# Optimization experiments

Hardware: AMD Instinct MI355X
Metric: run time of the kernel (lower is better)

## Reference

```python
import jax, jax.numpy as jnp
import numpy as np

NEG_SLOPE = 0.1

def mlp(x, w1, b1, w2, b2):
    # MLP(sizes): Linear -> LeakyReLU(0.1) -> Linear
    return jax.nn.leaky_relu(x @ w1 + b1, NEG_SLOPE) @ w2 + b2

def _seg_mean(vals, idx, n):
    s = jax.ops.segment_sum(vals, idx, num_segments=n)
    cnt = jax.ops.segment_sum(jnp.ones((vals.shape[0],), vals.dtype), idx, num_segments=n)
    return s / jnp.maximum(cnt, 1.0)[:, None]

def setup_inputs() -> dict:
    key = jax.random.key(0)
    ks = iter(jax.random.split(key, 40))
    N, F, H, E = 100000, 64, 128, 800000
    Ha = H // 2  # hidden_dim/2 = 64
    def lin(k, i, o):
        k1, k2 = jax.random.split(k)
        return (jax.random.normal(k1, (i, o), jnp.float32) * (1.0 / np.sqrt(i)),
                jax.random.normal(k2, (o,), jnp.float32) * 0.01)
    inp = {}
    inp['feat'] = jax.random.normal(next(ks), (N, F), jnp.float32)
    inp['pi_feat'] = jax.random.normal(next(ks), (N, 4), jnp.float32)
    inp['level'] = jax.random.uniform(next(ks), (N, 1), jnp.float32)
    inp['bit_position'] = jax.random.uniform(next(ks), (E, 1), jnp.float32)
    inp['is_po'] = jax.random.randint(next(ks), (N,), 0, 2, jnp.int32)
    inp['is_module'] = jax.random.randint(next(ks), (N,), 0, 2, jnp.int32)
    inp['src_m'] = jax.random.randint(next(ks), (E,), 0, N, jnp.int32)
    inp['dst_m'] = jax.random.randint(next(ks), (E,), 0, N, jnp.int32)
    inp['src_g'] = jax.random.randint(next(ks), (E,), 0, N, jnp.int32)
    inp['dst_g'] = jax.random.randint(next(ks), (E,), 0, N, jnp.int32)
    # mlp_pi: 4 -> H/2 -> H
    inp['pi_w1'], inp['pi_b1'] = lin(next(ks), 4, Ha)
    inp['pi_w2'], inp['pi_b2'] = lin(next(ks), Ha, H)
    # mlp_neigh_module: H + F + 1 -> H/2 -> H
    inp['nm_w1'], inp['nm_b1'] = lin(next(ks), H + F + 1, Ha)
    inp['nm_w2'], inp['nm_b2'] = lin(next(ks), Ha, H)
    # mlp_neigh_gate: H + F -> H/2 -> H
    inp['ng_w1'], inp['ng_b1'] = lin(next(ks), H + F, Ha)
    inp['ng_w2'], inp['ng_b2'] = lin(next(ks), Ha, H)
    # mlp_global: 1 -> H/2 -> H
    inp['g_w1'], inp['g_b1'] = lin(next(ks), 1, Ha)
    inp['g_w2'], inp['g_b2'] = lin(next(ks), Ha, H)
    # mlp_out: 2H -> H -> 1
    inp['o_w1'], inp['o_b1'] = lin(next(ks), 2 * H, H)
    inp['o_w2'], inp['o_b2'] = lin(next(ks), H, 1)
    return inp

def reference(feat, pi_feat, level, bit_position,
              pi_w1, pi_b1, pi_w2, pi_b2,
              nm_w1, nm_b1, nm_w2, nm_b2,
              ng_w1, ng_b1, ng_w2, ng_b2,
              g_w1, g_b1, g_w2, g_b2,
              o_w1, o_b1, o_w2, o_b2,
              is_po, is_module, src_m, dst_m, src_g, dst_g):
    N = feat.shape[0]
    # PI init embedding (mlp_pi)
    h0 = mlp(pi_feat, pi_w1, pi_b1, pi_w2, pi_b2)            # [N, H]
    # module-edge message passing: m = src h, pos = bit_position; mean reduce
    m = h0[src_m]                                            # [E, H] irregular gather
    neigh_m = _seg_mean(m, dst_m, N)                         # [N, H]
    pos_m = _seg_mean(bit_position, dst_m, N)                # [N, 1]
    # nodes_func_module, agg_choice==0: cat(neigh, pos, feat) -> mlp_neigh_module
    h_m = mlp(jnp.concatenate([neigh_m, pos_m, feat], axis=1), nm_w1, nm_b1, nm_w2, nm_b2)
    # gate-edge message passing
    neigh_g = _seg_mean(h0[src_g], dst_g, N)                 # [N, H]
    h_g = mlp(jnp.concatenate([neigh_g, feat], axis=1), ng_w1, ng_b1, ng_w2, ng_b2)
    # ReLU on non-PO nodes only
    keep = (is_po != 1)[:, None]
    h_m = jnp.where(keep, jax.nn.relu(h_m), h_m)
    h_g = jnp.where(keep, jax.nn.relu(h_g), h_g)
    # per-node-type update (hetero apply_nodes)
    h = jnp.where((is_module == 1)[:, None], h_m, h_g)       # [N, H]
    # global branch + readout
    hg = mlp(level, g_w1, g_b1, g_w2, g_b2)                  # [N, H]
    out = mlp(jnp.concatenate([h, hg], axis=1), o_w1, o_b1, o_w2, o_b2)  # [N, 1]
    return out
```

## Files before the change

### kernel.cpp

```cpp
#include <hip/hip_runtime.h>

typedef __bf16 bf16x8 __attribute__((ext_vector_type(8)));
typedef float f32x4 __attribute__((ext_vector_type(4)));
typedef unsigned short u16;
typedef unsigned int u32;
typedef unsigned long long u64;

__device__ __forceinline__ u16 f2b(float f) {
  return __builtin_bit_cast(u16, (__bf16)f);
}
__device__ __forceinline__ float b2f_lo(u32 pk) {
  return __builtin_bit_cast(float, pk << 16);
}
__device__ __forceinline__ float b2f_hi(u32 pk) {
  return __builtin_bit_cast(float, pk & 0xffff0000u);
}
__device__ __forceinline__ float leaky(float x) { return x > 0.f ? x : 0.1f * x; }
__device__ __forceinline__ f32x4 mfma16(bf16x8 a, bf16x8 b, f32x4 c) {
  return __builtin_amdgcn_mfma_f32_16x16x32_bf16(a, b, c, 0, 0, 0);
}

#define P64 72
#define P128 136
#define CAP 16
#define RSTRIDE 32

#define PREPB 32
#define SBLK 256
#define PBLK 224

__global__ __launch_bounds__(256) void k_init(
    const float* nm_w1, const float* ng_w1, const float* pi_w2, const float* pi_b2,
    const int* is_module,
    u16* wt_yc, float* bias_y, u16* wt_f1m, u16* wt_f1g,
    int* rec, int* spillcnt, u32* mbits, int N) {
  int i = blockIdx.x * 256 + threadIdx.x;
  if (i < 9216) {
    int ty = i / 4608, rem = i % 4608, n = rem / P64, k = rem % P64;
    float v = 0.f;
    if (k < 64) {
      const float* w1 = ty ? ng_w1 : nm_w1;
      for (int t = 0; t < 128; t++) v += pi_w2[k * 128 + t] * w1[t * 64 + n];
    }
    wt_yc[i] = f2b(v);
    return;
  }
  i -= 9216;
  if (i < 128) {
    int ty = i >> 6, n = i & 63;
    const float* w1 = ty ? ng_w1 : nm_w1;
    float v = 0.f;
    for (int t = 0; t < 128; t++) v += pi_b2[t] * w1[t * 64 + n];
    bias_y[i] = v;
    return;
  }
  i -= 128;
  if (i < 4608) {
    int n = i / P64, k = i % P64;
    wt_f1m[i] = f2b(k < 64 ? nm_w1[(129 + k) * 64 + n] : 0.f);
    return;
  }
  i -= 4608;
  if (i < 4608) {
    int n = i / P64, k = i % P64;
    wt_f1g[i] = f2b(k < 64 ? ng_w1[(128 + k) * 64 + n] : 0.f);
    return;
  }
  i -= 4608;
  {
    int n = i;
    int lane = threadIdx.x & 63;
    bool v = (n < N) && (is_module[n] == 1);
    u64 b = __ballot(v);
    if (n < N) {
      rec[(size_t)n * RSTRIDE] = 0;
      rec[(size_t)n * RSTRIDE + 1] = 0;
      if (lane == 0) mbits[n >> 5] = (u32)b;
      if (lane == 32) mbits[n >> 5] = (u32)(b >> 32);
    }
    if (n == 0) *spillcnt = 0;
  }
}

__global__ __launch_bounds__(512) void k_mid(
    const int* src_m, const int* dst_m, const int* src_g, const int* dst_g,
    const u32* mbits, const float* bitpos, int* rec, u64* spill, int* spillcnt,
    int E,
    const float* pf, const float* feat, const float* pi_w1, const float* pi_b1,
    const u16* wt_yc_g, const float* bias_y, const u16* wt_f1m_g, const u16* wt_f1g_g,
    const float* nm_b1, const float* ng_b1, u16* y0, u16* f1,
    const float* nm_w1, const float* nm_w2, const float* ng_w2,
    const float* o_w1, const float* o_b1, const float* g_w2, const float* g_b2,
    u16* wt2m, u16* wt2g, u16* wt_oh, u16* gt, float* bp, float* w_pos, int N) {
  __shared__ __align__(16) u16 wyc[2][64 * P64];
  __shared__ __align__(16) u16 wf[2][64 * P64];
  __shared__ __align__(16) u16 tbuf[8][16 * P64];

  if (blockIdx.x < PREPB) {
    const int TOTAL = 9216 + 9216 + 17408 + 9216 + 128 + 64;
    for (int it = blockIdx.x * 512 + threadIdx.x; it < TOTAL; it += PREPB * 512) {
      int i = it;
      if (i < 9216) {
        int n = i / P64, k = i % P64;
        wt2m[i] = f2b(k < 64 ? nm_w2[k * 128 + n] : 0.f);
        continue;
      }
      i -= 9216;
      if (i < 9216) {
        int n = i / P64, k = i % P64;
        wt2g[i] = f2b(k < 64 ? ng_w2[k * 128 + n] : 0.f);
        continue;
      }
      i -= 9216;
      if (i < 17408) {
        int n = i / P128, k = i % P128;
        wt_oh[i] = f2b(k < 128 ? o_w1[k * 128 + n] : 0.f);
        continue;
      }
      i -= 17408;
      if (i < 9216) {
        int n = i / P64, k = i % P64;
        float v = 0.f;
        if (k < 64)
          for (int t = 0; t < 128; t++) v += g_w2[k * 128 + t] * o_w1[(128 + t) * 128 + n];
        gt[i] = f2b(v);
        continue;
      }
      i -= 9216;
      if (i < 128) {
        float s = o_b1[i];
        for (int t = 0; t < 128; t++) s += g_b2[t] * o_w1[(128 + t) * 128 + i];
        bp[i] = s;
        continue;
      }
      i -= 128;
      w_pos[i] = nm_w1[128 * 64 + i];
    }
    return;
  }

  if (blockIdx.x < PREPB + SBLK) {
    int tid = (blockIdx.x - PREPB) * 512 + threadIdx.x;
    const int STR = SBLK * 512;
    for (int v0 = tid; v0 < E; v0 += STR * 4) {
      int dd[8], ss[8];
      float bb[8];
      bool el[8];
#pragma unroll
      for (int k = 0; k < 4; k++) {
        int vt = v0 + k * STR;
        bool vv = vt < E;
#pragma unroll
        for (int j = 0; j < 2; j++) {
          int x = k * 2 + j;
          el[x] = false;
          dd[x] = 0; ss[x] = 0; bb[x] = 0.f;
          if (vv) {
            int e = vt * 2 + j;
            int d = (e < E) ? dst_m[e] : dst_g[e - E];
            dd[x] = d;
            bool bit = (mbits[d >> 5] >> (d & 31)) & 1;
            el[x] = (e < E) ? bit : !bit;
            if (el[x]) {
              if (e < E) { ss[x] = src_m[e]; bb[x] = bitpos[e]; }
              else ss[x] = src_g[e - E];
            }
          }
        }
      }
      int cc[8];
#pragma unroll
      for (int x = 0; x < 8; x++)
        if (el[x]) cc[x] = atomicAdd(&rec[(size_t)dd[x] * RSTRIDE], 1);
#pragma unroll
      for (int x = 0; x < 8; x++) {
        if (!el[x]) continue;
        int vt = v0 + (x >> 1) * STR;
        int e = vt * 2 + (x & 1);
        int d = dd[x], s = ss[x], c = cc[x];
        if (e < E) {
          if (c < CAP) {
            int bp12 = (int)(bb[x] * 4096.f);
            if (bp12 > 4095) bp12 = 4095;
            rec[(size_t)d * RSTRIDE + 2 + c] = (s << 12) | bp12;
          } else {
            int p = atomicAdd(spillcnt, 1);
            spill[p] = ((u64)(u32)d << 32) | (u32)s;
            atomicAdd((float*)&rec[(size_t)d * RSTRIDE + 1], bb[x]);
          }
        } else {
          if (c < CAP) {
            rec[(size_t)d * RSTRIDE + 2 + c] = s << 12;
          } else {
            int p = atomicAdd(spillcnt, 1);
            spill[p] = ((u64)(u32)d << 32) | (u32)s;
          }
        }
      }
    }
    return;
  }

  int pb = blockIdx.x - PREPB - SBLK;
  for (int i = threadIdx.x; i < 2304; i += 512) {
    ((u32*)wyc[0])[i] = ((const u32*)wt_yc_g)[i];
    ((u32*)wyc[1])[i] = ((const u32*)wt_yc_g)[2304 + i];
    ((u32*)wf[0])[i] = ((const u32*)wt_f1m_g)[i];
    ((u32*)wf[1])[i] = ((const u32*)wt_f1g_g)[i];
  }

  int lane = threadIdx.x & 63, wv = threadIdx.x >> 6;
  int lid = lane & 15, q = lane >> 4;

  bf16x8 w1f[4];
#pragma unroll
  for (int nt = 0; nt < 4; nt++) {
    bf16x8 f;
#pragma unroll
    for (int j = 0; j < 8; j++) {
      int k = q * 8 + j;
      f[j] = (__bf16)((k < 4) ? pi_w1[k * 64 + nt * 16 + lid] : 0.f);
    }
    w1f[nt] = f;
  }
  __syncthreads();

  int nbat = (N + 15) >> 4;
  for (int b0 = pb * 8; b0 < nbat; b0 += PBLK * 8) {
    int b = b0 + wv;
    int batch = b < nbat ? b : nbat - 1;
    int id = batch * 16 + lid;
    if (id >= N) id = N - 1;

    bf16x8 a;
#pragma unroll
    for (int j = 0; j < 8; j++)
      a[j] = (__bf16)((q == 0 && j < 4) ? pf[(size_t)id * 4 + j] : 0.f);
    f32x4 z1[4];
#pragma unroll
    for (int nt = 0; nt < 4; nt++) {
      f32x4 c = {0.f, 0.f, 0.f, 0.f};
      z1[nt] = mfma16(a, w1f[nt], c);
    }
    __syncthreads();
#pragma unroll
    for (int nt = 0; nt < 4; nt++) {
      float bb = pi_b1[nt * 16 + lid];
#pragma unroll
      for (int r = 0; r < 4; r++)
        tbuf[wv][(q * 4 + r) * P64 + nt * 16 + lid] = f2b(leaky(z1[nt][r] + bb));
    }
    __syncthreads();
    bf16x8 a20 = *(const bf16x8*)&tbuf[wv][lid * P64 + q * 8];
    bf16x8 a21 = *(const bf16x8*)&tbuf[wv][lid * P64 + 32 + q * 8];

    int idr_[4];
#pragma unroll
    for (int r = 0; r < 4; r++) {
      int ii = batch * 16 + q * 4 + r;
      idr_[r] = ii < N ? ii : N - 1;
    }

#pragma unroll
    for (int ty = 0; ty < 2; ty++) {
#pragma unroll
      for (int nt = 0; nt < 4; nt++) {
        f32x4 c = {0.f, 0.f, 0.f, 0.f};
        c = mfma16(a20, *(const bf16x8*)&wyc[ty][(nt * 16 + lid) * P64 + q * 8], c);
        c = mfma16(a21, *(const bf16x8*)&wyc[ty][(nt * 16 + lid) * P64 + 32 + q * 8], c);
        float by = bias_y[ty * 64 + nt * 16 + lid];
#pragma unroll
        for (int r = 0; r < 4; r++)
          y0[(size_t)idr_[r] * 128 + ty * 64 + nt * 16 + lid] = f2b(c[r] + by);
      }
    }

    bf16x8 af[2];
#pragma unroll
    for (int kt = 0; kt < 2; kt++) {
      const float4* p = (const float4*)(feat + (size_t)id * 64 + kt * 32 + q * 8);
      float4 xa = p[0], xb = p[1];
      bf16x8 f;
      f[0] = (__bf16)xa.x; f[1] = (__bf16)xa.y; f[2] = (__bf16)xa.z; f[3] = (__bf16)xa.w;
      f[4] = (__bf16)xb.x; f[5] = (__bf16)xb.y; f[6] = (__bf16)xb.z; f[7] = (__bf16)xb.w;
      af[kt] = f;
    }
#pragma unroll
    for (int nt = 0; nt < 4; nt++) {
      f32x4 cm = {0.f, 0.f, 0.f, 0.f}, cg = {0.f, 0.f, 0.f, 0.f};
#pragma unroll
      for (int kt = 0; kt < 2; kt++) {
        cm = mfma16(af[kt], *(const bf16x8*)&wf[0][(nt * 16 + lid) * P64 + kt * 32 + q * 8], cm);
        cg = mfma16(af[kt], *(const bf16x8*)&wf[1][(nt * 16 + lid) * P64 + kt * 32 + q * 8], cg);
      }
      float bm = nm_b1[nt * 16 + lid], bg = ng_b1[nt * 16 + lid];
#pragma unroll
      for (int r = 0; r < 4; r++) {
        int idr = idr_[r];
        bool mod = (mbits[idr >> 5] >> (idr & 31)) & 1;
        f1[(size_t)idr * 64 + nt * 16 + lid] = f2b(mod ? cm[r] + bm : cg[r] + bg);
      }
    }
  }
}

__global__ __launch_bounds__(256) void k_gather(const u16* y0, const int* rec,
                                                const u64* spill, const int* spillcnt,
                                                const u32* mbits, const u16* f1,
                                                const float* w_pos, u16* z1a, int N) {
  int n = (blockIdx.x * 256 + threadIdx.x) >> 6;
  int lane = threadIdx.x & 63;
  if (n >= N) return;
  bool mod = (mbits[n >> 5] >> (n & 31)) & 1;
  int g = lane >> 4, l16 = lane & 15;
  int rv = (lane < 18) ? rec[(size_t)n * RSTRIDE + lane] : 0;
  int cnt = __shfl(rv, 0);
  float pspill = __builtin_bit_cast(float, __shfl(rv, 1));
  int inl = cnt < CAP ? cnt : CAP;
  float myb = 0.f;
  if (mod && lane >= 2 && lane < 18 && (lane - 2) < inl)
    myb = (float)(rv & 4095) * (1.f / 4096.f);
  const u32* yrow = (const u32*)y0;
  int halfo = mod ? 0 : 32;
  float a00 = 0.f, a01 = 0.f, a10 = 0.f, a11 = 0.f;
  for (int j = 0; j < inl; j += 4) {
    int e = j + g;
    if (e < inl) {
      int s = (int)(((u32)__shfl(rv, 2 + e)) >> 12);
      u64 pk = *(const u64*)(yrow + (size_t)s * 64 + halfo + 2 * l16);
      u32 p0 = (u32)pk, p1 = (u32)(pk >> 32);
      a00 += b2f_lo(p0); a01 += b2f_hi(p0);
      a10 += b2f_lo(p1); a11 += b2f_hi(p1);
    }
  }
  if (cnt > CAP) {
    int sc = *spillcnt;
    int idx = 0;
    for (int base = 0; base < sc; base += 64) {
      int i = base + lane;
      u64 ent = (i < sc) ? spill[i] : 0xffffffffffffffffull;
      bool m = ((int)(ent >> 32) == n);
      u64 bal = __ballot(m);
      int slo = (int)(ent & 0xffffffffu);
      while (bal) {
        int l = __ffsll((long long)bal) - 1;
        bal &= bal - 1;
        int s = __shfl(slo, l);
        if ((idx & 3) == g) {
          u64 pk = *(const u64*)(yrow + (size_t)s * 64 + halfo + 2 * l16);
          u32 p0 = (u32)pk, p1 = (u32)(pk >> 32);
          a00 += b2f_lo(p0); a01 += b2f_hi(p0);
          a10 += b2f_lo(p1); a11 += b2f_hi(p1);
        }
        idx++;
      }
    }
  }
  a00 += __shfl_xor(a00, 16); a00 += __shfl_xor(a00, 32);
  a01 += __shfl_xor(a01, 16); a01 += __shfl_xor(a01, 32);
  a10 += __shfl_xor(a10, 16); a10 += __shfl_xor(a10, 32);
  a11 += __shfl_xor(a11, 16); a11 += __shfl_xor(a11, 32);
#pragma unroll
  for (int off = 1; off < 64; off <<= 1) myb += __shfl_xor(myb, off);
  float psum = pspill + myb;
  float inv = 1.f / (float)(cnt > 1 ? cnt : 1);
  if (lane < 16) {
    u64 fp2 = *(const u64*)(((const u32*)f1) + (size_t)n * 32 + 2 * l16);
    u32 f0 = (u32)fp2, f1v = (u32)(fp2 >> 32);
    float z00 = a00 * inv + b2f_lo(f0);
    float z01 = a01 * inv + b2f_hi(f0);
    float z10 = a10 * inv + b2f_lo(f1v);
    float z11 = a11 * inv + b2f_hi(f1v);
    if (mod) {
      float pm = psum * inv;
      float4 wp = ((const float4*)w_pos)[l16];
      z00 += pm * wp.x; z01 += pm * wp.y;
      z10 += pm * wp.z; z11 += pm * wp.w;
    }
    u32 r0 = (u32)f2b(leaky(z00)) | ((u32)f2b(leaky(z01)) << 16);
    u32 r1 = (u32)f2b(leaky(z10)) | ((u32)f2b(leaky(z11)) << 16);
    *(u64*)(((u32*)z1a) + (size_t)n * 32 + 2 * l16) = ((u64)r1 << 32) | r0;
  }
}

__global__ __launch_bounds__(512) void k_tail(const u16* z1a, const u16* wt2m_g,
                                              const u16* wt2g_g, const float* nm_b2,
                                              const float* ng_b2, const u32* mbits,
                                              const int* is_po, const float* level,
                                              const float* g_w1, const float* g_b1,
                                              const u16* wt_oh_g, const u16* gt_g,
                                              const float* bp_g, const float* o_w2,
                                              const float* o_b2, float* out, int N) {
  __shared__ __align__(16) u16 w2[2][128 * P64];
  __shared__ __align__(16) u16 wt_oh[128 * P128];
  __shared__ __align__(16) u16 gt[128 * P64];
  __shared__ __align__(16) u16 tbuf[8][16 * P128];
  for (int i = threadIdx.x; i < 128 * P64 / 2; i += 512) {
    ((u32*)w2[0])[i] = ((const u32*)wt2m_g)[i];
    ((u32*)w2[1])[i] = ((const u32*)wt2g_g)[i];
    ((u32*)gt)[i] = ((const u32*)gt_g)[i];
  }
  for (int i = threadIdx.x; i < 128 * P128 / 2; i += 512)
    ((u32*)wt_oh)[i] = ((const u32*)wt_oh_g)[i];

  int lane = threadIdx.x & 63, wv = threadIdx.x >> 6;
  int lid = lane & 15, q = lane >> 4;
  int nbat = (N + 15) >> 4;

  float gw[2][8], gb[2][8];
#pragma unroll
  for (int kt = 0; kt < 2; kt++)
#pragma unroll
    for (int j = 0; j < 8; j++) {
      int k = kt * 32 + q * 8 + j;
      gw[kt][j] = g_w1[k];
      gb[kt][j] = g_b1[k];
    }
  float w2o[8], bpv[8];
#pragma unroll
  for (int nt = 0; nt < 8; nt++) {
    w2o[nt] = o_w2[nt * 16 + lid];
    bpv[nt] = bp_g[nt * 16 + lid];
  }
  float b2m[8], b2g[8];
#pragma unroll
  for (int nt = 0; nt < 8; nt++) {
    b2m[nt] = nm_b2[nt * 16 + lid];
    b2g[nt] = ng_b2[nt * 16 + lid];
  }
  float ob2 = o_b2[0];
  __syncthreads();

  for (int b0 = blockIdx.x * 8; b0 < nbat; b0 += gridDim.x * 8) {
    int b = b0 + wv;
    int batch = b < nbat ? b : nbat - 1;
    int id = batch * 16 + lid;
    if (id >= N) id = N - 1;

    bf16x8 a0 = *(const bf16x8*)(z1a + (size_t)id * 64 + q * 8);
    bf16x8 a1 = *(const bf16x8*)(z1a + (size_t)id * 64 + 32 + q * 8);
    bool mod_[4], kp_[4];
#pragma unroll
    for (int r = 0; r < 4; r++) {
      int ii = batch * 16 + q * 4 + r;
      if (ii >= N) ii = N - 1;
      mod_[r] = (mbits[ii >> 5] >> (ii & 31)) & 1;
      kp_[r] = (is_po[ii] != 1);
    }
    __syncthreads();
#pragma unroll
    for (int nt = 0; nt < 8; nt++) {
      f32x4 cm = {0.f, 0.f, 0.f, 0.f}, cg = {0.f, 0.f, 0.f, 0.f};
      cm = mfma16(a0, *(const bf16x8*)&w2[0][(nt * 16 + lid) * P64 + q * 8], cm);
      cm = mfma16(a1, *(const bf16x8*)&w2[0][(nt * 16 + lid) * P64 + 32 + q * 8], cm);
      cg = mfma16(a0, *(const bf16x8*)&w2[1][(nt * 16 + lid) * P64 + q * 8], cg);
      cg = mfma16(a1, *(const bf16x8*)&w2[1][(nt * 16 + lid) * P64 + 32 + q * 8], cg);
#pragma unroll
      for (int r = 0; r < 4; r++) {
        float v = mod_[r] ? cm[r] + b2m[nt] : cg[r] + b2g[nt];
        if (kp_[r]) v = fmaxf(v, 0.f);
        tbuf[wv][(q * 4 + r) * P128 + nt * 16 + lid] = f2b(v);
      }
    }
    __syncthreads();

    bf16x8 ah[4];
#pragma unroll
    for (int kt = 0; kt < 4; kt++)
      ah[kt] = *(const bf16x8*)&tbuf[wv][lid * P128 + kt * 32 + q * 8];
    float lv = level[id];
    bf16x8 ag[2];
#pragma unroll
    for (int kt = 0; kt < 2; kt++)
#pragma unroll
      for (int j = 0; j < 8; j++)
        ag[kt][j] = (__bf16)leaky(lv * gw[kt][j] + gb[kt][j]);

    f32x4 accv[8];
#pragma unroll
    for (int nt = 0; nt < 8; nt++) {
      f32x4 c = {0.f, 0.f, 0.f, 0.f};
#pragma unroll
      for (int kt = 0; kt < 4; kt++)
        c = mfma16(ah[kt], *(const bf16x8*)&wt_oh[(nt * 16 + lid) * P128 + kt * 32 + q * 8], c);
#pragma unroll
      for (int kt = 0; kt < 2; kt++)
        c = mfma16(ag[kt], *(const bf16x8*)&gt[(nt * 16 + lid) * P64 + kt * 32 + q * 8], c);
      accv[nt] = c;
    }
    float p[4];
#pragma unroll
    for (int r = 0; r < 4; r++) {
      float s = 0.f;
#pragma unroll
      for (int nt = 0; nt < 8; nt++) s += leaky(accv[nt][r] + bpv[nt]) * w2o[nt];
      p[r] = s;
    }
#pragma unroll
    for (int r = 0; r < 4; r++)
#pragma unroll
      for (int off = 1; off < 16; off <<= 1) p[r] += __shfl_xor(p[r], off, 16);
    if (lid == 0) {
#pragma unroll
      for (int r = 0; r < 4; r++) {
        int idr = batch * 16 + q * 4 + r;
        if (idr >= N) idr = N - 1;
        out[idr] = p[r] + ob2;
      }
    }
  }
}

extern "C" void kernel_launch(void* const* d_in, const int* in_sizes, int n_in,
                              void* d_out, int out_size, void* d_ws, size_t ws_size,
                              hipStream_t stream) {
  const float* feat = (const float*)d_in[0];
  const float* pi_feat = (const float*)d_in[1];
  const float* level = (const float*)d_in[2];
  const float* bitpos = (const float*)d_in[3];
  const int* is_po = (const int*)d_in[4];
  const int* is_module = (const int*)d_in[5];
  const int* src_m = (const int*)d_in[6];
  const int* dst_m = (const int*)d_in[7];
  const int* src_g = (const int*)d_in[8];
  const int* dst_g = (const int*)d_in[9];
  const float* pi_w1 = (const float*)d_in[10];
  const float* pi_b1 = (const float*)d_in[11];
  const float* pi_w2 = (const float*)d_in[12];
  const float* pi_b2 = (const float*)d_in[13];
  const float* nm_w1 = (const float*)d_in[14];
  const float* nm_b1 = (const float*)d_in[15];
  const float* nm_w2 = (const float*)d_in[16];
  const float* nm_b2 = (const float*)d_in[17];
  const float* ng_w1 = (const float*)d_in[18];
  const float* ng_b1 = (const float*)d_in[19];
  const float* ng_w2 = (const float*)d_in[20];
  const float* ng_b2 = (const float*)d_in[21];
  const float* g_w1 = (const float*)d_in[22];
  const float* g_b1 = (const float*)d_in[23];
  const float* g_w2 = (const float*)d_in[24];
  const float* g_b2 = (const float*)d_in[25];
  const float* o_w1 = (const float*)d_in[26];
  const float* o_b1 = (const float*)d_in[27];
  const float* o_w2 = (const float*)d_in[28];
  const float* o_b2 = (const float*)d_in[29];

  int N = in_sizes[0] / 64;
  int E = in_sizes[3];

  char* ws = (char*)d_ws;
  size_t off = 0;
  auto alloc = [&](size_t bytes) {
    char* p = ws + off;
    off += (bytes + 255) & ~(size_t)255;
    return p;
  };
  int* rec = (int*)alloc(((size_t)N * RSTRIDE + 64) * 4);
  int* spillcnt = (int*)alloc(16);
  u64* spill = (u64*)alloc((size_t)2 * E * 8);
  u32* mbits = (u32*)alloc((size_t)((N + 31) / 32) * 4);
  u16* y0 = (u16*)alloc((size_t)N * 128 * 2);
  u16* f1 = (u16*)alloc((size_t)N * 64 * 2);
  u16* z1a = (u16*)alloc((size_t)N * 64 * 2);
  u16* wt_yc = (u16*)alloc(9216 * 2);
  float* bias_y = (float*)alloc(128 * 4);
  u16* wt_f1m = (u16*)alloc(4608 * 2);
  u16* wt_f1g = (u16*)alloc(4608 * 2);
  float* w_pos = (float*)alloc(64 * 4);
  u16* wt2m = (u16*)alloc(9216 * 2);
  u16* wt2g = (u16*)alloc(9216 * 2);
  u16* wt_oh = (u16*)alloc(17408 * 2);
  u16* gt = (u16*)alloc(9216 * 2);
  float* bp = (float*)alloc(128 * 4);

  int init_items = 18560 + ((N + 63) & ~63);
  k_init<<<(init_items + 255) / 256, 256, 0, stream>>>(
      nm_w1, ng_w1, pi_w2, pi_b2, is_module,
      wt_yc, bias_y, wt_f1m, wt_f1g, rec, spillcnt, mbits, N);

  k_mid<<<PREPB + SBLK + PBLK, 512, 0, stream>>>(
      src_m, dst_m, src_g, dst_g, mbits, bitpos, rec, spill, spillcnt, E,
      pi_feat, feat, pi_w1, pi_b1, wt_yc, bias_y, wt_f1m, wt_f1g,
      nm_b1, ng_b1, y0, f1,
      nm_w1, nm_w2, ng_w2, o_w1, o_b1, g_w2, g_b2,
      wt2m, wt2g, wt_oh, gt, bp, w_pos, N);

  k_gather<<<(N * 64 + 255) / 256, 256, 0, stream>>>(
      y0, rec, spill, spillcnt, mbits, f1, w_pos, z1a, N);

  k_tail<<<256, 512, 0, stream>>>(z1a, wt2m, wt2g, nm_b2, ng_b2, mbits, is_po,
                                  level, g_w1, g_b1, wt_oh, gt, bp, o_w2, o_b2,
                                  (float*)d_out, N);
}
```

Before: 260.9 us.

## Fuse neighbor gather into tail kernel, keeping z1 activations in LDS

Merges the gather/mean-aggregation kernel into the tail MLP kernel. Each wave now gathers 16 nodes at once, with 4 lanes per node and 16-byte loads, and writes the first-layer activations to a per-wave LDS buffer instead of the z1a global array. It also removes the block-wide __syncthreads inside the loop, since each wave only touches its own LDS slices. This drops one launch and the z1a write and read-back. In exchange, gather parallelism is limited to the tail kernel's 256 persistent blocks, which may expose gather latency, and LDS use goes up, which may lower occupancy.

```diff
diff --git a/kernel.cpp b/kernel.cpp
--- a/kernel.cpp
+++ b/kernel.cpp
@@ -304,97 +304,18 @@
   }
 }
 
-__global__ __launch_bounds__(256) void k_gather(const u16* y0, const int* rec,
-                                                const u64* spill, const int* spillcnt,
-                                                const u32* mbits, const u16* f1,
-                                                const float* w_pos, u16* z1a, int N) {
-  int n = (blockIdx.x * 256 + threadIdx.x) >> 6;
-  int lane = threadIdx.x & 63;
-  if (n >= N) return;
-  bool mod = (mbits[n >> 5] >> (n & 31)) & 1;
-  int g = lane >> 4, l16 = lane & 15;
-  int rv = (lane < 18) ? rec[(size_t)n * RSTRIDE + lane] : 0;
-  int cnt = __shfl(rv, 0);
-  float pspill = __builtin_bit_cast(float, __shfl(rv, 1));
-  int inl = cnt < CAP ? cnt : CAP;
-  float myb = 0.f;
-  if (mod && lane >= 2 && lane < 18 && (lane - 2) < inl)
-    myb = (float)(rv & 4095) * (1.f / 4096.f);
-  const u32* yrow = (const u32*)y0;
-  int halfo = mod ? 0 : 32;
-  float a00 = 0.f, a01 = 0.f, a10 = 0.f, a11 = 0.f;
-  for (int j = 0; j < inl; j += 4) {
-    int e = j + g;
-    if (e < inl) {
-      int s = (int)(((u32)__shfl(rv, 2 + e)) >> 12);
-      u64 pk = *(const u64*)(yrow + (size_t)s * 64 + halfo + 2 * l16);
-      u32 p0 = (u32)pk, p1 = (u32)(pk >> 32);
-      a00 += b2f_lo(p0); a01 += b2f_hi(p0);
-      a10 += b2f_lo(p1); a11 += b2f_hi(p1);
-    }
-  }
-  if (cnt > CAP) {
-    int sc = *spillcnt;
-    int idx = 0;
-    for (int base = 0; base < sc; base += 64) {
-      int i = base + lane;
-      u64 ent = (i < sc) ? spill[i] : 0xffffffffffffffffull;
-      bool m = ((int)(ent >> 32) == n);
-      u64 bal = __ballot(m);
-      int slo = (int)(ent & 0xffffffffu);
-      while (bal) {
-        int l = __ffsll((long long)bal) - 1;
-        bal &= bal - 1;
-        int s = __shfl(slo, l);
-        if ((idx & 3) == g) {
-          u64 pk = *(const u64*)(yrow + (size_t)s * 64 + halfo + 2 * l16);
-          u32 p0 = (u32)pk, p1 = (u32)(pk >> 32);
-          a00 += b2f_lo(p0); a01 += b2f_hi(p0);
-          a10 += b2f_lo(p1); a11 += b2f_hi(p1);
-        }
-        idx++;
-      }
-    }
-  }
-  a00 += __shfl_xor(a00, 16); a00 += __shfl_xor(a00, 32);
-  a01 += __shfl_xor(a01, 16); a01 += __shfl_xor(a01, 32);
-  a10 += __shfl_xor(a10, 16); a10 += __shfl_xor(a10, 32);
-  a11 += __shfl_xor(a11, 16); a11 += __shfl_xor(a11, 32);
-#pragma unroll
-  for (int off = 1; off < 64; off <<= 1) myb += __shfl_xor(myb, off);
-  float psum = pspill + myb;
-  float inv = 1.f / (float)(cnt > 1 ? cnt : 1);
-  if (lane < 16) {
-    u64 fp2 = *(const u64*)(((const u32*)f1) + (size_t)n * 32 + 2 * l16);
-    u32 f0 = (u32)fp2, f1v = (u32)(fp2 >> 32);
-    float z00 = a00 * inv + b2f_lo(f0);
-    float z01 = a01 * inv + b2f_hi(f0);
-    float z10 = a10 * inv + b2f_lo(f1v);
-    float z11 = a11 * inv + b2f_hi(f1v);
-    if (mod) {
-      float pm = psum * inv;
-      float4 wp = ((const float4*)w_pos)[l16];
-      z00 += pm * wp.x; z01 += pm * wp.y;
-      z10 += pm * wp.z; z11 += pm * wp.w;
-    }
-    u32 r0 = (u32)f2b(leaky(z00)) | ((u32)f2b(leaky(z01)) << 16);
-    u32 r1 = (u32)f2b(leaky(z10)) | ((u32)f2b(leaky(z11)) << 16);
-    *(u64*)(((u32*)z1a) + (size_t)n * 32 + 2 * l16) = ((u64)r1 << 32) | r0;
-  }
-}
-
-__global__ __launch_bounds__(512) void k_tail(const u16* z1a, const u16* wt2m_g,
-                                              const u16* wt2g_g, const float* nm_b2,
-                                              const float* ng_b2, const u32* mbits,
-                                              const int* is_po, const float* level,
-                                              const float* g_w1, const float* g_b1,
-                                              const u16* wt_oh_g, const u16* gt_g,
-                                              const float* bp_g, const float* o_w2,
-                                              const float* o_b2, float* out, int N) {
+__global__ __launch_bounds__(512) void k_gt2(
+    const u16* y0, const int* rec, const u64* spill, const int* spillcnt,
+    const u32* mbits, const u16* f1, const float* w_pos,
+    const u16* wt2m_g, const u16* wt2g_g, const float* nm_b2, const float* ng_b2,
+    const int* is_po, const float* level, const float* g_w1, const float* g_b1,
+    const u16* wt_oh_g, const u16* gt_g, const float* bp_g, const float* o_w2,
+    const float* o_b2, float* out, int N) {
   __shared__ __align__(16) u16 w2[2][128 * P64];
   __shared__ __align__(16) u16 wt_oh[128 * P128];
   __shared__ __align__(16) u16 gt[128 * P64];
   __shared__ __align__(16) u16 tbuf[8][16 * P128];
+  __shared__ __align__(16) u32 zl[8][16][36];
   for (int i = threadIdx.x; i < 128 * P64 / 2; i += 512) {
     ((u32*)w2[0])[i] = ((const u32*)wt2m_g)[i];
     ((u32*)w2[1])[i] = ((const u32*)wt2g_g)[i];
@@ -405,6 +326,7 @@
 
   int lane = threadIdx.x & 63, wv = threadIdx.x >> 6;
   int lid = lane & 15, q = lane >> 4;
+  int g4 = lane >> 2, c = lane & 3, base4 = lane & ~3;
   int nbat = (N + 15) >> 4;
 
   float gw[2][8], gb[2][8];
@@ -431,14 +353,126 @@
   float ob2 = o_b2[0];
   __syncthreads();
 
+  const u32* yrow = (const u32*)y0;
+
   for (int b0 = blockIdx.x * 8; b0 < nbat; b0 += gridDim.x * 8) {
     int b = b0 + wv;
     int batch = b < nbat ? b : nbat - 1;
+
+    {
+      int n = batch * 16 + g4;
+      if (n >= N) n = N - 1;
+      bool mod = (mbits[n >> 5] >> (n & 31)) & 1;
+      int halfo = mod ? 0 : 32;
+      const int* rbase = rec + (size_t)n * RSTRIDE;
+      int4 r4 = ((const int4*)rbase)[c];
+      int e16 = 0, e17 = 0;
+      if (c == 1) { e16 = rbase[16]; e17 = rbase[17]; }
+      int cnt = __shfl(r4.x, base4);
+      float pspill = __builtin_bit_cast(float, __shfl(r4.y, base4));
+      int inl = cnt < CAP ? cnt : CAP;
+      float myb = 0.f;
+      float alo[8], ahi[8];
+#pragma unroll
+      for (int m = 0; m < 8; m++) { alo[m] = 0.f; ahi[m] = 0.f; }
+#pragma unroll
+      for (int j = 0; j < 16; j++) {
+        int slot;
+        if (j < 14) {
+          const int own = (j + 2) >> 2, comp = (j + 2) & 3;
+          int v = comp == 0 ? r4.x : comp == 1 ? r4.y : comp == 2 ? r4.z : r4.w;
+          slot = __shfl(v, base4 + own);
+        } else {
+          slot = __shfl(j == 14 ? e16 : e17, base4 + 1);
+        }
+        if (j < inl) {
+          if (mod) myb += (float)(slot & 4095) * (1.f / 4096.f);
+          int s = (int)(((u32)slot) >> 12);
+          const u32* rowp = yrow + (size_t)s * 64 + halfo + c * 8;
+          uint4 pa = *(const uint4*)rowp;
+          uint4 pb = *(const uint4*)(rowp + 4);
+          alo[0] += b2f_lo(pa.x); ahi[0] += b2f_hi(pa.x);
+          alo[1] += b2f_lo(pa.y); ahi[1] += b2f_hi(pa.y);
+          alo[2] += b2f_lo(pa.z); ahi[2] += b2f_hi(pa.z);
+          alo[3] += b2f_lo(pa.w); ahi[3] += b2f_hi(pa.w);
+          alo[4] += b2f_lo(pb.x); ahi[4] += b2f_hi(pb.x);
+          alo[5] += b2f_lo(pb.y); ahi[5] += b2f_hi(pb.y);
+          alo[6] += b2f_lo(pb.z); ahi[6] += b2f_hi(pb.z);
+          alo[7] += b2f_lo(pb.w); ahi[7] += b2f_hi(pb.w);
+        }
+      }
+      u64 over = __ballot(c == 0 && cnt > CAP);
+      if (over) {
+        int sc = *spillcnt;
+        while (over) {
+          int bit = __ffsll((long long)over) - 1;
+          over &= over - 1;
+          int gsel = bit >> 2;
+          int n_t = __shfl(n, bit);
+          int halfo_t = __shfl(halfo, bit);
+          for (int bb = 0; bb < sc; bb += 64) {
+            int i = bb + lane;
+            u64 ent = (i < sc) ? spill[i] : 0xffffffffffffffffull;
+            bool m = ((int)(ent >> 32) == n_t);
+            u64 bal = __ballot(m);
+            int slo = (int)(ent & 0xffffffffu);
+            while (bal) {
+              int l = __ffsll((long long)bal) - 1;
+              bal &= bal - 1;
+              int s = __shfl(slo, l);
+              if (g4 == gsel) {
+                const u32* rowp = yrow + (size_t)s * 64 + halfo_t + c * 8;
+                uint4 pa = *(const uint4*)rowp;
+                uint4 pb = *(const uint4*)(rowp + 4);
+                alo[0] += b2f_lo(pa.x); ahi[0] += b2f_hi(pa.x);
+                alo[1] += b2f_lo(pa.y); ahi[1] += b2f_hi(pa.y);
+                alo[2] += b2f_lo(pa.z); ahi[2] += b2f_hi(pa.z);
+                alo[3] += b2f_lo(pa.w); ahi[3] += b2f_hi(pa.w);
+                alo[4] += b2f_lo(pb.x); ahi[4] += b2f_hi(pb.x);
+                alo[5] += b2f_lo(pb.y); ahi[5] += b2f_hi(pb.y);
+                alo[6] += b2f_lo(pb.z); ahi[6] += b2f_hi(pb.z);
+                alo[7] += b2f_lo(pb.w); ahi[7] += b2f_hi(pb.w);
+              }
+            }
+          }
+        }
+      }
+      float psum = pspill + myb;
+      float inv = 1.f / (float)(cnt > 1 ? cnt : 1);
+      float pm = mod ? psum * inv : 0.f;
+      const u32* f1p = ((const u32*)f1) + (size_t)n * 32 + c * 8;
+      uint4 fa = *(const uint4*)f1p;
+      uint4 fb = *(const uint4*)(f1p + 4);
+      const float4* wp4 = (const float4*)w_pos;
+      float4 wpa = wp4[c * 4 + 0], wpb = wp4[c * 4 + 1];
+      float4 wpc = wp4[c * 4 + 2], wpd = wp4[c * 4 + 3];
+      u32 zr[8];
+#pragma unroll
+      for (int m = 0; m < 8; m++) {
+        u32 fw = (m == 0) ? fa.x : (m == 1) ? fa.y : (m == 2) ? fa.z : (m == 3) ? fa.w
+               : (m == 4) ? fb.x : (m == 5) ? fb.y : (m == 6) ? fb.z : fb.w;
+        float z0 = alo[m] * inv + b2f_lo(fw);
+        float z1v = ahi[m] * inv + b2f_hi(fw);
+        if (mod) {
+          float4 w4 = ((m >> 1) == 0) ? wpa : ((m >> 1) == 1) ? wpb
+                    : ((m >> 1) == 2) ? wpc : wpd;
+          float wx = (m & 1) ? w4.z : w4.x;
+          float wy = (m & 1) ? w4.w : w4.y;
+          z0 += pm * wx;
+          z1v += pm * wy;
+        }
+        zr[m] = (u32)f2b(leaky(z0)) | ((u32)f2b(leaky(z1v)) << 16);
+      }
+      u32* zp = &zl[wv][g4][c * 8];
+      *(uint4*)zp = make_uint4(zr[0], zr[1], zr[2], zr[3]);
+      *(uint4*)(zp + 4) = make_uint4(zr[4], zr[5], zr[6], zr[7]);
+    }
+
     int id = batch * 16 + lid;
     if (id >= N) id = N - 1;
-
-    bf16x8 a0 = *(const bf16x8*)(z1a + (size_t)id * 64 + q * 8);
-    bf16x8 a1 = *(const bf16x8*)(z1a + (size_t)id * 64 + 32 + q * 8);
+    const u16* zrow = (const u16*)zl[wv][lid];
+    bf16x8 a0 = *(const bf16x8*)&zrow[q * 8];
+    bf16x8 a1 = *(const bf16x8*)&zrow[32 + q * 8];
     bool mod_[4], kp_[4];
 #pragma unroll
     for (int r = 0; r < 4; r++) {
@@ -447,7 +481,6 @@
       mod_[r] = (mbits[ii >> 5] >> (ii & 31)) & 1;
       kp_[r] = (is_po[ii] != 1);
     }
-    __syncthreads();
 #pragma unroll
     for (int nt = 0; nt < 8; nt++) {
       f32x4 cm = {0.f, 0.f, 0.f, 0.f}, cg = {0.f, 0.f, 0.f, 0.f};
@@ -462,7 +495,6 @@
         tbuf[wv][(q * 4 + r) * P128 + nt * 16 + lid] = f2b(v);
       }
     }
-    __syncthreads();
 
     bf16x8 ah[4];
 #pragma unroll
@@ -479,14 +511,14 @@
     f32x4 accv[8];
 #pragma unroll
     for (int nt = 0; nt < 8; nt++) {
-      f32x4 c = {0.f, 0.f, 0.f, 0.f};
+      f32x4 cc = {0.f, 0.f, 0.f, 0.f};
 #pragma unroll
       for (int kt = 0; kt < 4; kt++)
-        c = mfma16(ah[kt], *(const bf16x8*)&wt_oh[(nt * 16 + lid) * P128 + kt * 32 + q * 8], c);
+        cc = mfma16(ah[kt], *(const bf16x8*)&wt_oh[(nt * 16 + lid) * P128 + kt * 32 + q * 8], cc);
 #pragma unroll
       for (int kt = 0; kt < 2; kt++)
-        c = mfma16(ag[kt], *(const bf16x8*)&gt[(nt * 16 + lid) * P64 + kt * 32 + q * 8], c);
-      accv[nt] = c;
+        cc = mfma16(ag[kt], *(const bf16x8*)&gt[(nt * 16 + lid) * P64 + kt * 32 + q * 8], cc);
+      accv[nt] = cc;
     }
     float p[4];
 #pragma unroll
@@ -561,7 +593,6 @@
   u32* mbits = (u32*)alloc((size_t)((N + 31) / 32) * 4);
   u16* y0 = (u16*)alloc((size_t)N * 128 * 2);
   u16* f1 = (u16*)alloc((size_t)N * 64 * 2);
-  u16* z1a = (u16*)alloc((size_t)N * 64 * 2);
   u16* wt_yc = (u16*)alloc(9216 * 2);
   float* bias_y = (float*)alloc(128 * 4);
   u16* wt_f1m = (u16*)alloc(4608 * 2);
@@ -585,10 +616,8 @@
       nm_w1, nm_w2, ng_w2, o_w1, o_b1, g_w2, g_b2,
       wt2m, wt2g, wt_oh, gt, bp, w_pos, N);
 
-  k_gather<<<(N * 64 + 255) / 256, 256, 0, stream>>>(
-      y0, rec, spill, spillcnt, mbits, f1, w_pos, z1a, N);
-
-  k_tail<<<256, 512, 0, stream>>>(z1a, wt2m, wt2g, nm_b2, ng_b2, mbits, is_po,
-                                  level, g_w1, g_b1, wt_oh, gt, bp, o_w2, o_b2,
-                                  (float*)d_out, N);
-}
+  k_gt2<<<256, 512, 0, stream>>>(
+      y0, rec, spill, spillcnt, mbits, f1, w_pos,
+      wt2m, wt2g, nm_b2, ng_b2, is_po, level, g_w1, g_b1,
+      wt_oh, gt, bp, o_w2, o_b2, (float*)d_out, N);
+}
```

Result: faster. 248.7 us (-4.7%).
